# Kernel tuning notes

Hardware: AMD Instinct MI355X
Metric: run time of the kernel (lower is better)

## Reference

```python
import jax, jax.numpy as jnp
import numpy as np

N, E, DIN, GB, GD, LB, LD, G = 50000, 640000, 64, 128, 4, 256, 2, 1024


def setup_inputs() -> dict:
    key = jax.random.key(0)
    ks = jax.random.split(key, 20)
    p = lambda k, shape: (jax.random.normal(k, shape, dtype=jnp.float32) * 0.05)
    return {
        "x": jax.random.normal(ks[0], (N, DIN), dtype=jnp.float32),
        "edge_index": jax.random.randint(ks[1], (2, E), 0, N, dtype=jnp.int64),
        "batch": jnp.sort(jax.random.randint(ks[2], (N,), 0, G, dtype=jnp.int64)),
        "num_graphs": G,
        "W0": p(ks[3], (DIN, GB)), "b0": p(ks[4], (GB,)),
        "Wg": p(ks[5], (GD, GB, GB)), "bg": p(ks[6], (GD, GB)),
        "gamma_g": jnp.ones((GD, GB), jnp.float32), "beta_g": jnp.zeros((GD, GB), jnp.float32),
        "Wl0": p(ks[7], (GB, LB)), "bl0": p(ks[8], (LB,)),
        "Wl": p(ks[9], (LD, LB, LB)), "bl": p(ks[10], (LD, LB)),
        "gamma_l": jnp.ones((LD, LB), jnp.float32), "beta_l": jnp.zeros((LD, LB), jnp.float32),
        "Wout": p(ks[11], (LB, 2)), "bout": p(ks[12], (2,)),
    }


def reference(x, edge_index, batch, num_graphs, W0, b0, Wg, bg, gamma_g, beta_g,
              Wl0, bl0, Wl, bl, gamma_l, beta_l, Wout, bout):
    n = x.shape[0]
    src, dst = edge_index[0], edge_index[1]
    # GCN degree normalization with self loops: deg = 1 + in-degree
    deg = jax.ops.segment_sum(jnp.ones(src.shape[0], x.dtype), dst, num_segments=n) + 1.0
    dinv = jax.lax.rsqrt(deg)                 # deg^{-1/2}
    enorm = dinv[src] * dinv[dst]             # [E] edge norm
    snorm = dinv * dinv                       # [N] self-loop norm (deg^{-1})

    def gcn(h, W, b):
        hw = h @ W                                            # [N, GB]
        agg = jax.ops.segment_sum(hw[src] * enorm[:, None], dst, num_segments=n)
        return agg + hw * snorm[:, None] + b

    def bn(h, g, bt):  # training-mode batchnorm (biased var), eps=1e-5
        m = h.mean(0)
        v = h.var(0)
        return (h - m) * jax.lax.rsqrt(v + 1e-5) * g + bt

    h = jax.nn.relu(gcn(x, W0, b0))
    for i in range(Wg.shape[0]):
        h = jax.nn.relu(bn(gcn(h, Wg[i], bg[i]), gamma_g[i], beta_g[i]))
    # global_add_pool
    hp = jax.ops.segment_sum(h, batch, num_segments=num_graphs)  # [G, GB]
    h = jax.nn.relu(hp @ Wl0 + bl0)
    for i in range(Wl.shape[0]):
        h = jax.nn.relu(bn(h @ Wl[i] + bl[i], gamma_l[i], beta_l[i]))
    return h @ Wout + bout
```

## Files before the change

kernel.cpp:

```cpp
#include <hip/hip_runtime.h>

#define NN 50000
#define EE 640000
#define DINv 64
#define GBv 128
#define GDv 4
#define LBv 256
#define LDv 2
#define GGv 1024

#define NB 196
#define BCAP 4096
#define BTILE 4096
#define NBT ((EE + BTILE - 1) / BTILE)

#define NTILES ((NN + 63) / 64)
#define UPN (NN * 16)
#define CONVN (DINv * GBv + GDv * GBv * GBv)
#define ZEXT 320

typedef _Float16 f16x8 __attribute__((ext_vector_type(8)));
typedef float f32x4 __attribute__((ext_vector_type(4)));

__device__ __forceinline__ float h2f(ushort u) {
  union { ushort u; _Float16 h; } x;
  x.u = u;
  return (float)x.h;
}
__device__ __forceinline__ ushort f2h(float f) {
  union { ushort u; _Float16 h; } x;
  x.h = (_Float16)f;
  return x.u;
}


__global__ __launch_bounds__(256) void k_bucket(const int* __restrict__ ei,
                                                int* __restrict__ bcnt,
                                                uint* __restrict__ bkt) {
  __shared__ int lcnt[NB];
  __shared__ int lbase[NB];
  __shared__ int gbase[NB];
  __shared__ int ls[256];
  __shared__ uint stage[BTILE];
  __shared__ ushort sb[BTILE];
  int tid = threadIdx.x;
  int t0 = blockIdx.x * BTILE;
  int cnt = min(BTILE, EE - t0);
  for (int i = tid; i < NB; i += 256) lcnt[i] = 0;
  __syncthreads();

  uint en[16];
  int bb[16], rk[16];
  int nper = (cnt + 255) >> 8;
  for (int k = 0; k < nper; k++) {
    int e = k * 256 + tid;
    if (e < cnt) {
      int src = ei[t0 + e];
      int dst = ei[EE + t0 + e];
      int b = dst >> 8;
      en[k] = ((uint)src << 8) | (uint)(dst & 255);
      bb[k] = b;
      rk[k] = atomicAdd(&lcnt[b], 1);
    } else {
      bb[k] = -1;
    }
  }
  __syncthreads();

  int v = (tid < NB) ? lcnt[tid] : 0;
  ls[tid] = v;
  __syncthreads();
  for (int off = 1; off < 256; off <<= 1) {
    int t = (tid >= off) ? ls[tid - off] : 0;
    __syncthreads();
    ls[tid] += t;
    __syncthreads();
  }
  if (tid < NB) {
    lbase[tid] = ls[tid] - v;
    gbase[tid] = atomicAdd(&bcnt[tid], v);
  }
  __syncthreads();

  for (int k = 0; k < nper; k++) {
    if (bb[k] >= 0) {
      int slot = lbase[bb[k]] + rk[k];
      stage[slot] = en[k];
      sb[slot] = (ushort)bb[k];
    }
  }
  __syncthreads();

  for (int i = tid; i < cnt; i += 256) {
    int b = sb[i];
    bkt[(size_t)b * BCAP + gbase[b] + (i - lbase[b])] = stage[i];
  }
}


__global__ __launch_bounds__(256) void k_csr(const uint* __restrict__ bkt,
                                             const int* __restrict__ bcnt,
                                             int* __restrict__ offs,
                                             float* __restrict__ dinv,
                                             int* __restrict__ col,
                                             int* __restrict__ deg,
                                             int* __restrict__ ghist) {
  __shared__ int lhist[256];
  __shared__ int lofs[256];
  __shared__ int lcur[256];
  __shared__ int lsb[256];
  __shared__ int lh2[64];
  int b = blockIdx.x;
  int tid = threadIdx.x;
  int bv = (tid < NB) ? bcnt[tid] : 0;
  lsb[tid] = bv;
  lhist[tid] = 0;
  if (tid < 64) lh2[tid] = 0;
  __syncthreads();
  for (int off = 1; off < 256; off <<= 1) {
    int t = (tid >= off) ? lsb[tid - off] : 0;
    __syncthreads();
    lsb[tid] += t;
    __syncthreads();
  }
  int cnt = bcnt[b];
  int rawbase = lsb[b] - cnt;
  int pbase = ((rawbase + 7) & ~7) + b * 4096;
  const uint* B = bkt + (size_t)b * BCAP;
  for (int i = tid; i < cnt; i += 256) atomicAdd(&lhist[B[i] & 255], 1);
  __syncthreads();
  int v = lhist[tid];
  int pv = (v + 7) & ~7;
  lofs[tid] = pv;
  __syncthreads();
  for (int off = 1; off < 256; off <<= 1) {
    int t = (tid >= off) ? lofs[tid - off] : 0;
    __syncthreads();
    lofs[tid] += t;
    __syncthreads();
  }
  int excl = lofs[tid] - pv;
  int n = b * 256 + tid;
  if (n < NN) {
    offs[n] = pbase + excl;
    dinv[n] = rsqrtf((float)(v + 1));
    deg[n] = v;
    atomicAdd(&lh2[min(v, 63)], 1);
    for (int k = v; k < pv; k++) col[pbase + excl + k] = NN;
  }
  lcur[tid] = excl;
  __syncthreads();
  if (tid < 64 && lh2[tid]) atomicAdd(&ghist[tid], lh2[tid]);
  if (b == 0 && tid == 0) dinv[NN] = 0.f;
  for (int i = tid; i < cnt; i += 256) {
    uint e = B[i];
    int p = atomicAdd(&lcur[e & 255], 1);
    col[pbase + p] = (int)(e >> 8);
  }
}


__global__ __launch_bounds__(256) void k_dperm(const int* __restrict__ deg,
                                               const int* __restrict__ ghist,
                                               int* __restrict__ gcur,
                                               int* __restrict__ perm) {
  __shared__ int lhist[64];
  __shared__ int lbase[64];
  int tid = threadIdx.x;
  if (tid < 64) lhist[tid] = 0;
  __syncthreads();
  int n = blockIdx.x * 256 + tid;
  int d = 0, rk = 0;
  if (n < NN) {
    d = min(deg[n], 63);
    rk = atomicAdd(&lhist[d], 1);
  }
  __syncthreads();
  if (tid < 64) {
    int s = 0;
    for (int i = tid + 1; i < 64; i++) s += ghist[i];
    if (lhist[tid]) lbase[tid] = s + atomicAdd(&gcur[tid], lhist[tid]);
  }
  __syncthreads();
  if (n < NN) perm[lbase[d] + rk] = n;
}


__global__ __launch_bounds__(256) void k_prep(const float* __restrict__ x,
                                              const float* __restrict__ dinv,
                                              const float* __restrict__ W0,
                                              const float* __restrict__ Wg,
                                              ushort* __restrict__ u,
                                              ushort* __restrict__ Wt0,
                                              ushort* __restrict__ Wtg,
                                              ushort* __restrict__ g1,
                                              ushort* __restrict__ g3) {
  int idx = blockIdx.x * 256 + threadIdx.x;
  if (idx < UPN) {
    int n = idx >> 4;
    float4 v = ((const float4*)x)[idx];
    float d = dinv[n];
    union { ushort us[4]; uint2 q; } o;
    o.us[0] = f2h(v.x * d);
    o.us[1] = f2h(v.y * d);
    o.us[2] = f2h(v.z * d);
    o.us[3] = f2h(v.w * d);
    ((uint2*)u)[idx] = o.q;
  } else {
    int j = idx - UPN;
    if (j < DINv * GBv) {
      int c = j >> 6, k = j & 63;
      Wt0[j] = f2h(W0[k * GBv + c]);
    } else if (j < CONVN) {
      int e = j - DINv * GBv;
      int i = e >> 14, rem = e & 16383;
      int c = rem >> 7, k = rem & 127;
      Wtg[e] = f2h(Wg[i * GBv * GBv + k * GBv + c]);
    } else if (j < CONVN + ZEXT) {
      int z = j - CONVN;
      if (z < 64) u[(size_t)NN * DINv + z] = 0;
      else if (z < 192) g1[(size_t)NN * GBv + (z - 64)] = 0;
      else g3[(size_t)NN * GBv + (z - 192)] = 0;
    }
  }
}


__global__ __launch_bounds__(256) void k_bn(const ushort* __restrict__ G,
                                            const float* __restrict__ st,
                                            const float* __restrict__ gamma,
                                            const float* __restrict__ beta,
                                            const float* __restrict__ dinv,
                                            ushort* __restrict__ Gt) {
  __shared__ float sS[128], sT[128];
  int tid = threadIdx.x;
  if (tid < 128) {
    float mu = st[tid] * (1.f / NN);
    float var = st[128 + tid] * (1.f / NN) - mu * mu;
    float s = rsqrtf(var + 1e-5f) * gamma[tid];
    sS[tid] = s;
    sT[tid] = beta[tid] - mu * s;
  }
  __syncthreads();
  int idx = blockIdx.x * 256 + tid;
  if (idx < NN * 16) {
    int n = idx >> 4, c0 = (idx & 15) * 8;
    float dv = dinv[n];
    union { uint4 v4; ushort us[8]; } in, o;
    in.v4 = ((const uint4*)G)[idx];
#pragma unroll
    for (int v = 0; v < 8; v++)
      o.us[v] = f2h(fmaxf(h2f(in.us[v]) * sS[c0 + v] + sT[c0 + v], 0.f) * dv);
    ((uint4*)Gt)[idx] = o.v4;
  }
}


template <int K, bool STATS, bool OUTF>
__global__ __launch_bounds__(512, 2) void k_layer(const ushort* __restrict__ Gin,
                                                  const int* __restrict__ col,
                                                  const int* __restrict__ offs,
                                                  const int* __restrict__ deg,
                                                  const float* __restrict__ dinv,
                                                  const int* __restrict__ perm,
                                                  const ushort* __restrict__ Wt,
                                                  const float* __restrict__ bias,
                                                  float* __restrict__ stG,
                                                  ushort* __restrict__ Gout) {
  constexpr int VEC = K / 16;
  constexpr int KP = K + 8;
  constexpr int CP = 136;
  __shared__ __attribute__((aligned(16))) _Float16 sA[64 * 136];
  __shared__ float sB[128];
  __shared__ float ssum[128], ssq[128];
  __shared__ float sDn[64];
  _Float16* sC = sA;
  int tid = threadIdx.x;

  if (tid < 128) {
    sB[tid] = bias[tid];
    if constexpr (STATS) {
      ssum[tid] = 0.f;
      ssq[tid] = 0.f;
    }
  }

  int w = tid >> 6, lane = tid & 63;
  int quad = lane >> 4, m = lane & 15;
  int row0 = blockIdx.x * 64;

  union U { uint4 v4; uint2 v2; ushort us[8]; };
  auto loadrow = [&](int s) {
    U u;
    const ushort* p = Gin + (long)s * K + m * VEC;
    if constexpr (VEC == 8) u.v4 = *(const uint4*)p;
    else u.v2 = *(const uint2*)p;
    return u;
  };

  for (int rnd = 0; rnd < 2; rnd++) {
    int r = rnd * 32 + w * 4 + quad;
    int idx = row0 + r;
    float acc[VEC];
#pragma unroll
    for (int v = 0; v < VEC; v++) acc[v] = 0.f;
    float dn = 0.f;
    if (idx < NN) {
      int n = perm[idx];
      dn = dinv[n];
      auto addrow = [&](U u) {
#pragma unroll
        for (int v = 0; v < VEC; v++) acc[v] += h2f(u.us[v]);
      };

      int s0 = offs[n];
      int pcnt = (deg[n] + 7) & ~7;
      const int* cp = col + s0;

      U uself = loadrow(n);
      addrow(uself);
      for (int j = 0; j < pcnt; j += 8) {
        int4 c0 = *(const int4*)(cp + j);
        int4 c1 = *(const int4*)(cp + j + 4);
        U uu[8];
        uu[0] = loadrow(c0.x);
        uu[1] = loadrow(c0.y);
        uu[2] = loadrow(c0.z);
        uu[3] = loadrow(c0.w);
        uu[4] = loadrow(c1.x);
        uu[5] = loadrow(c1.y);
        uu[6] = loadrow(c1.z);
        uu[7] = loadrow(c1.w);
#pragma unroll
        for (int t = 0; t < 8; t++) addrow(uu[t]);
      }
    }
    if constexpr (OUTF) {
      if (m == 0) sDn[r] = dn;
    }
    U o;
#pragma unroll
    for (int v = 0; v < VEC; v++) o.us[v] = f2h(acc[v] * dn);
    _Float16* ap = &sA[r * KP + m * VEC];
    if constexpr (VEC == 8) *(uint4*)ap = o.v4;
    else *(uint2*)ap = o.v2;
  }
  __syncthreads();

  int wr = w >> 1, wc = w & 1;
  f32x4 acc2[4];
#pragma unroll
  for (int ct = 0; ct < 4; ct++) acc2[ct] = (f32x4){0.f, 0.f, 0.f, 0.f};
  const _Float16* pa = &sA[(16 * wr + m) * KP + quad * 8];
#pragma unroll
  for (int ks = 0; ks < K; ks += 32) {
    f16x8 a = *(const f16x8*)(pa + ks);
#pragma unroll
    for (int ct = 0; ct < 4; ct++) {
      int c = wc * 64 + ct * 16 + m;
      f16x8 bfr = *(const f16x8*)((const _Float16*)Wt + (size_t)c * K + ks + quad * 8);
      acc2[ct] = __builtin_amdgcn_mfma_f32_16x16x32_f16(a, bfr, acc2[ct], 0, 0, 0);
    }
  }

  int crow = 16 * wr + quad * 4;
  float ps[4], pq[4];
  if constexpr (STATS) {
#pragma unroll
    for (int ct = 0; ct < 4; ct++) {
      int c = wc * 64 + ct * 16 + m;
      float bb = sB[c];
      ps[ct] = 0.f;
      pq[ct] = 0.f;
#pragma unroll
      for (int r = 0; r < 4; r++) {
        if (row0 + crow + r < NN) {
          float g = acc2[ct][r] + bb;
          ps[ct] += g;
          pq[ct] += g * g;
        }
      }
    }
  }
  __syncthreads();

  float dvr[4];
  if constexpr (OUTF) {
#pragma unroll
    for (int r = 0; r < 4; r++) dvr[r] = sDn[crow + r];
  }
#pragma unroll
  for (int ct = 0; ct < 4; ct++) {
    int c = wc * 64 + ct * 16 + m;
    float bb = sB[c];
#pragma unroll
    for (int r = 0; r < 4; r++) {
      float y = acc2[ct][r] + bb;
      if constexpr (OUTF) y = fmaxf(y, 0.f) * dvr[r];
      sC[(crow + r) * CP + c] = (_Float16)y;
    }
  }
  __syncthreads();

  {
    int r = tid >> 3;
    int c0 = (tid & 7) * 16;
    int idx2 = row0 + r;
    if (idx2 < NN) {
      int node = perm[idx2];
      const uint4* srcp = (const uint4*)&sC[r * CP + c0];
      uint4* dst = (uint4*)(Gout + (long)node * 128 + c0);
      dst[0] = srcp[0];
      dst[1] = srcp[1];
    }
  }

  if constexpr (STATS) {
#pragma unroll
    for (int ct = 0; ct < 4; ct++) {
      float s = ps[ct], q = pq[ct];
      s += __shfl_xor(s, 16);
      q += __shfl_xor(q, 16);
      s += __shfl_xor(s, 32);
      q += __shfl_xor(q, 32);
      if (quad == 0) {
        atomicAdd(&ssum[wc * 64 + ct * 16 + m], s);
        atomicAdd(&ssq[wc * 64 + ct * 16 + m], q);
      }
    }
    __syncthreads();
    if (tid < 128) {
      int c = (tid + blockIdx.x * 8) & 127;
      atomicAdd(&stG[c], ssum[c]);
      atomicAdd(&stG[128 + c], ssq[c]);
    }
  }
}


__global__ __launch_bounds__(128) void k_pool2(const ushort* __restrict__ G,
                                               const float* __restrict__ st,
                                               const float* __restrict__ gamma,
                                               const float* __restrict__ beta,
                                               const int* __restrict__ batch,
                                               float* __restrict__ hp) {
  __shared__ int sse[2];
  int g = blockIdx.x;
  int c = threadIdx.x;
  if (c < 2) {
    int key = g + c;
    int lo = 0, hi = NN;
    while (lo < hi) {
      int mid = (lo + hi) >> 1;
      if (batch[mid] < key) lo = mid + 1;
      else hi = mid;
    }
    sse[c] = lo;
  }
  __syncthreads();
  int s = sse[0], e = sse[1];
  float m = st[c] * (1.f / NN);
  float v = st[128 + c] * (1.f / NN) - m * m;
  float sc = rsqrtf(v + 1e-5f) * gamma[c];
  float tc = beta[c] - m * sc;
  float a0 = 0.f, a1 = 0.f, a2 = 0.f, a3 = 0.f;
  int n = s;
  for (; n + 3 < e; n += 4) {
    float g0 = h2f(G[(long)(n + 0) * 128 + c]);
    float g1 = h2f(G[(long)(n + 1) * 128 + c]);
    float g2 = h2f(G[(long)(n + 2) * 128 + c]);
    float g3 = h2f(G[(long)(n + 3) * 128 + c]);
    a0 += fmaxf(g0 * sc + tc, 0.f);
    a1 += fmaxf(g1 * sc + tc, 0.f);
    a2 += fmaxf(g2 * sc + tc, 0.f);
    a3 += fmaxf(g3 * sc + tc, 0.f);
  }
  for (; n < e; n++) a0 += fmaxf(h2f(G[(long)n * 128 + c]) * sc + tc, 0.f);
  hp[(long)g * 128 + c] = (a0 + a1) + (a2 + a3);
}


__global__ void k_colstats(const float* __restrict__ X, int rows, float* __restrict__ st) {
  int c = threadIdx.x;
  int C = blockDim.x;
  float s = 0.f, q = 0.f;
  for (int r = blockIdx.x; r < rows; r += gridDim.x) {
    float v = X[(long)r * C + c];
    s += v;
    q += v * v;
  }
  atomicAdd(&st[c], s);
  atomicAdd(&st[C + c], q);
}


template <int KIN, int MODE>
__global__ __launch_bounds__(256) void k_fc(const float* __restrict__ X,
                                            const float* __restrict__ W,
                                            const float* __restrict__ b,
                                            const float* __restrict__ st,
                                            const float* __restrict__ gamma,
                                            const float* __restrict__ beta,
                                            float* __restrict__ Y) {
  __shared__ float sx[KIN];
  int g = blockIdx.x;
  int c = threadIdx.x;
  for (int k = c; k < KIN; k += 256) {
    float v = X[(long)g * KIN + k];
    if constexpr (MODE == 2) {
      float m = st[k] * (1.f / GGv);
      float var = st[KIN + k] * (1.f / GGv) - m * m;
      v = fmaxf((v - m) * rsqrtf(var + 1e-5f) * gamma[k] + beta[k], 0.f);
    }
    sx[k] = v;
  }
  __syncthreads();
  float acc = b[c];
#pragma unroll 8
  for (int k = 0; k < KIN; k++) acc += sx[k] * W[(long)k * 256 + c];
  Y[(long)g * 256 + c] = (MODE == 0) ? fmaxf(acc, 0.f) : acc;
}

__global__ __launch_bounds__(256) void k_out(const float* __restrict__ X,
                                             const float* __restrict__ st,
                                             const float* __restrict__ gamma,
                                             const float* __restrict__ beta,
                                             const float* __restrict__ Wout,
                                             const float* __restrict__ bout,
                                             float* __restrict__ out) {
  int g = blockIdx.x * 4 + (threadIdx.x >> 6);
  int l = threadIdx.x & 63;
  float a0 = 0.f, a1 = 0.f;
  for (int k = l; k < LBv; k += 64) {
    float z = X[(long)g * LBv + k];
    float m = st[k] * (1.f / GGv);
    float var = st[LBv + k] * (1.f / GGv) - m * m;
    float x = fmaxf((z - m) * rsqrtf(var + 1e-5f) * gamma[k] + beta[k], 0.f);
    a0 += x * Wout[2 * k];
    a1 += x * Wout[2 * k + 1];
  }
  for (int off = 32; off > 0; off >>= 1) {
    a0 += __shfl_down(a0, off);
    a1 += __shfl_down(a1, off);
  }
  if (l == 0) {
    out[2 * g] = a0 + bout[0];
    out[2 * g + 1] = a1 + bout[1];
  }
}


extern "C" void kernel_launch(void* const* d_in, const int* in_sizes, int n_in,
                              void* d_out, int out_size, void* d_ws, size_t ws_size,
                              hipStream_t stream) {
  const float* x = (const float*)d_in[0];
  const int* ei = (const int*)d_in[1];
  const int* batch = (const int*)d_in[2];
  const float* W0 = (const float*)d_in[4];
  const float* b0 = (const float*)d_in[5];
  const float* Wg = (const float*)d_in[6];
  const float* bg = (const float*)d_in[7];
  const float* gamma_g = (const float*)d_in[8];
  const float* beta_g = (const float*)d_in[9];
  const float* Wl0 = (const float*)d_in[10];
  const float* bl0 = (const float*)d_in[11];
  const float* Wl = (const float*)d_in[12];
  const float* bl = (const float*)d_in[13];
  const float* gamma_l = (const float*)d_in[14];
  const float* beta_l = (const float*)d_in[15];
  const float* Wout = (const float*)d_in[16];
  const float* bout = (const float*)d_in[17];
  float* out = (float*)d_out;

  char* w = (char*)d_ws;
  auto alloc = [&](size_t bytes) {
    void* p = (void*)w;
    w += (bytes + 255) & ~(size_t)255;
    return p;
  };
  int* bcnt = (int*)alloc((size_t)NB * 4);
  float* stAll = (float*)alloc((size_t)(4 * 256 + 2 * 512) * 4);
  int* ghist = (int*)alloc((size_t)64 * 4);
  int* gcur = (int*)alloc((size_t)64 * 4);
  size_t zspan = (char*)w - (char*)bcnt;
  uint* bkt = (uint*)alloc((size_t)NB * BCAP * 4);
  int* offs = (int*)alloc((size_t)(NN + 1) * 4);
  int* col = (int*)alloc((size_t)(EE + NB * 4096 + 8192) * 4);
  float* dinv = (float*)alloc((size_t)(NN + 1) * 4);
  int* deg = (int*)alloc((size_t)NN * 4);
  int* perm = (int*)alloc((size_t)NN * 4);
  ushort* u = (ushort*)alloc((size_t)(NN + 1) * DINv * 2);
  ushort* g1 = (ushort*)alloc((size_t)(NN + 1) * GBv * 2);
  ushort* g2 = (ushort*)alloc((size_t)(NN + 1) * GBv * 2);
  ushort* g3 = (ushort*)alloc((size_t)(NN + 1) * GBv * 2);
  ushort* Wt0 = (ushort*)alloc((size_t)DINv * GBv * 2);
  ushort* Wtg = (ushort*)alloc((size_t)GDv * GBv * GBv * 2);
  float* hp = (float*)alloc((size_t)GGv * GBv * 4);
  float* m1 = (float*)alloc((size_t)GGv * LBv * 4);
  float* m2 = (float*)alloc((size_t)GGv * LBv * 4);

  float* stg = stAll;
  float* sth0 = stAll + 4 * 256;
  float* sth1 = sth0 + 512;

  hipMemsetAsync(bcnt, 0, zspan, stream);

  k_bucket<<<NBT, 256, 0, stream>>>(ei, bcnt, bkt);
  k_csr<<<NB, 256, 0, stream>>>(bkt, bcnt, offs, dinv, col, deg, ghist);
  k_dperm<<<NB, 256, 0, stream>>>(deg, ghist, gcur, perm);
  k_prep<<<(UPN + CONVN + ZEXT + 255) / 256, 256, 0, stream>>>(x, dinv, W0, Wg, u, Wt0,
                                                               Wtg, g1, g3);

  const int BNG = (NN * 16 + 255) / 256;

  k_layer<64, false, true><<<NTILES, 512, 0, stream>>>(u, col, offs, deg, dinv, perm,
                                                       Wt0, b0, nullptr, g1);
  k_layer<128, true, false><<<NTILES, 512, 0, stream>>>(g1, col, offs, deg, dinv, perm,
                                                        Wtg, bg, stg, g2);
  for (int i = 1; i < GDv; i++) {
    k_bn<<<BNG, 256, 0, stream>>>(g2, stg + (size_t)(i - 1) * 256,
                                  gamma_g + (size_t)(i - 1) * GBv,
                                  beta_g + (size_t)(i - 1) * GBv, dinv, g3);
    k_layer<128, true, false><<<NTILES, 512, 0, stream>>>(
        g3, col, offs, deg, dinv, perm, Wtg + (size_t)i * GBv * GBv,
        bg + (size_t)i * GBv, stg + (size_t)i * 256, g2);
  }

  k_pool2<<<GGv, 128, 0, stream>>>(g2, stg + 3 * 256, gamma_g + 3 * GBv, beta_g + 3 * GBv,
                                   batch, hp);

  k_fc<GBv, 0><<<GGv, 256, 0, stream>>>(hp, Wl0, bl0, nullptr, nullptr, nullptr, m1);
  k_fc<LBv, 1><<<GGv, 256, 0, stream>>>(m1, Wl, bl, nullptr, nullptr, nullptr, m2);
  k_colstats<<<256, LBv, 0, stream>>>(m2, GGv, sth0);
  k_fc<LBv, 2><<<GGv, 256, 0, stream>>>(m2, Wl + (size_t)LBv * LBv, bl + LBv, sth0,
                                        gamma_l, beta_l, m1);
  k_colstats<<<256, LBv, 0, stream>>>(m1, GGv, sth1);
  k_out<<<GGv / 4, 256, 0, stream>>>(m1, sth1, gamma_l + LBv, beta_l + LBv, Wout, bout, out);
}
```

Measured before the change: 451.0 us.

## Interleave degree-sorted node permutation across tiles to balance gather work

The degree-sorted permutation is strided across tiles so that each 64-row tile gets a mix of high- and low-degree nodes. Previously each tile held nodes of similar degree, so tile costs were very uneven. Leftover slots in the last tiles are padded with a dummy node whose degree, dinv and offset are zero, and bounds checks now test for that sentinel. Rows in a wave still differ in degree, so lanes within a wave may diverge more in the neighbour loop.

Result: slower. 462.2 us (+2.5%).

```diff
diff --git a/kernel.cpp b/kernel.cpp
--- a/kernel.cpp
+++ b/kernel.cpp
@@ -18,6 +18,8 @@
 #define UPN (NN * 16)
 #define CONVN (DINv * GBv + GDv * GBv * GBv)
 #define ZEXT 320
+#define HT0 (NN - 63 * NTILES)
+#define NHOLES (NTILES - HT0)
 
 typedef _Float16 f16x8 __attribute__((ext_vector_type(8)));
 typedef float f32x4 __attribute__((ext_vector_type(4)));
@@ -151,7 +153,11 @@
   lcur[tid] = excl;
   __syncthreads();
   if (tid < 64 && lh2[tid]) atomicAdd(&ghist[tid], lh2[tid]);
-  if (b == 0 && tid == 0) dinv[NN] = 0.f;
+  if (b == 0 && tid == 0) {
+    dinv[NN] = 0.f;
+    deg[NN] = 0;
+    offs[NN] = 0;
+  }
   for (int i = tid; i < cnt; i += 256) {
     uint e = B[i];
     int p = atomicAdd(&lcur[e & 255], 1);
@@ -182,7 +188,10 @@
     if (lhist[tid]) lbase[tid] = s + atomicAdd(&gcur[tid], lhist[tid]);
   }
   __syncthreads();
-  if (n < NN) perm[lbase[d] + rk] = n;
+  if (n < NN) {
+    int R = lbase[d] + rk;
+    perm[((R % NTILES) << 6) + R / NTILES] = n;
+  }
 }
 
 
@@ -194,7 +203,8 @@
                                               ushort* __restrict__ Wt0,
                                               ushort* __restrict__ Wtg,
                                               ushort* __restrict__ g1,
-                                              ushort* __restrict__ g3) {
+                                              ushort* __restrict__ g3,
+                                              int* __restrict__ perm) {
   int idx = blockIdx.x * 256 + threadIdx.x;
   if (idx < UPN) {
     int n = idx >> 4;
@@ -221,6 +231,9 @@
       if (z < 64) u[(size_t)NN * DINv + z] = 0;
       else if (z < 192) g1[(size_t)NN * GBv + (z - 64)] = 0;
       else g3[(size_t)NN * GBv + (z - 192)] = 0;
+    } else if (j < CONVN + ZEXT + NHOLES) {
+      int t = j - (CONVN + ZEXT);
+      perm[(HT0 + t) * 64 + 63] = NN;
     }
   }
 }
@@ -300,14 +313,12 @@
 
   for (int rnd = 0; rnd < 2; rnd++) {
     int r = rnd * 32 + w * 4 + quad;
-    int idx = row0 + r;
+    int n = perm[row0 + r];
+    float dn = dinv[n];
     float acc[VEC];
 #pragma unroll
     for (int v = 0; v < VEC; v++) acc[v] = 0.f;
-    float dn = 0.f;
-    if (idx < NN) {
-      int n = perm[idx];
-      dn = dinv[n];
+    {
       auto addrow = [&](U u) {
 #pragma unroll
         for (int v = 0; v < VEC; v++) acc[v] += h2f(u.us[v]);
@@ -335,9 +346,7 @@
         for (int t = 0; t < 8; t++) addrow(uu[t]);
       }
     }
-    if constexpr (OUTF) {
-      if (m == 0) sDn[r] = dn;
-    }
+    if (m == 0) sDn[r] = dn;
     U o;
 #pragma unroll
     for (int v = 0; v < VEC; v++) o.us[v] = f2h(acc[v] * dn);
@@ -364,6 +373,10 @@
   }
 
   int crow = 16 * wr + quad * 4;
+  float dval[4];
+#pragma unroll
+  for (int r = 0; r < 4; r++) dval[r] = sDn[crow + r];
+
   float ps[4], pq[4];
   if constexpr (STATS) {
 #pragma unroll
@@ -374,7 +387,7 @@
       pq[ct] = 0.f;
 #pragma unroll
       for (int r = 0; r < 4; r++) {
-        if (row0 + crow + r < NN) {
+        if (dval[r] > 0.f) {
           float g = acc2[ct][r] + bb;
           ps[ct] += g;
           pq[ct] += g * g;
@@ -384,11 +397,6 @@
   }
   __syncthreads();
 
-  float dvr[4];
-  if constexpr (OUTF) {
-#pragma unroll
-    for (int r = 0; r < 4; r++) dvr[r] = sDn[crow + r];
-  }
 #pragma unroll
   for (int ct = 0; ct < 4; ct++) {
     int c = wc * 64 + ct * 16 + m;
@@ -396,7 +404,7 @@
 #pragma unroll
     for (int r = 0; r < 4; r++) {
       float y = acc2[ct][r] + bb;
-      if constexpr (OUTF) y = fmaxf(y, 0.f) * dvr[r];
+      if constexpr (OUTF) y = fmaxf(y, 0.f) * dval[r];
       sC[(crow + r) * CP + c] = (_Float16)y;
     }
   }
@@ -405,9 +413,8 @@
   {
     int r = tid >> 3;
     int c0 = (tid & 7) * 16;
-    int idx2 = row0 + r;
-    if (idx2 < NN) {
-      int node = perm[idx2];
+    int node = perm[row0 + r];
+    if (node < NN) {
       const uint4* srcp = (const uint4*)&sC[r * CP + c0];
       uint4* dst = (uint4*)(Gout + (long)node * 128 + c0);
       dst[0] = srcp[0];
@@ -587,8 +594,8 @@
   int* offs = (int*)alloc((size_t)(NN + 1) * 4);
   int* col = (int*)alloc((size_t)(EE + NB * 4096 + 8192) * 4);
   float* dinv = (float*)alloc((size_t)(NN + 1) * 4);
-  int* deg = (int*)alloc((size_t)NN * 4);
-  int* perm = (int*)alloc((size_t)NN * 4);
+  int* deg = (int*)alloc((size_t)(NN + 1) * 4);
+  int* perm = (int*)alloc((size_t)(NTILES * 64) * 4);
   ushort* u = (ushort*)alloc((size_t)(NN + 1) * DINv * 2);
   ushort* g1 = (ushort*)alloc((size_t)(NN + 1) * GBv * 2);
   ushort* g2 = (ushort*)alloc((size_t)(NN + 1) * GBv * 2);
@@ -608,8 +615,8 @@
   k_bucket<<<NBT, 256, 0, stream>>>(ei, bcnt, bkt);
   k_csr<<<NB, 256, 0, stream>>>(bkt, bcnt, offs, dinv, col, deg, ghist);
   k_dperm<<<NB, 256, 0, stream>>>(deg, ghist, gcur, perm);
-  k_prep<<<(UPN + CONVN + ZEXT + 255) / 256, 256, 0, stream>>>(x, dinv, W0, Wg, u, Wt0,
-                                                               Wtg, g1, g3);
+  k_prep<<<(UPN + CONVN + ZEXT + NHOLES + 255) / 256, 256, 0, stream>>>(
+      x, dinv, W0, Wg, u, Wt0, Wtg, g1, g3, perm);
 
   const int BNG = (NN * 16 + 255) / 256;
 
```
